# Optimization experiments

Hardware: AMD Instinct MI355X
Metric: run time of the kernel (lower is better)

Reference implementation:

```python
import jax, jax.numpy as jnp
import numpy as np

N_NODES = 100000
N_EDGES = 1200000
N_GRAPHS = 256
IN_C, HID_C, OUT_C = 5, 64, 2


def gcn_conv(x, src, dst, W, b, n_nodes):
    """PyG GCNConv: h = x@W; add self-loops; deg from target col (edge weight 1);
    norm = deg^{-1/2}[src]*deg^{-1/2}[dst]; scatter-add messages into dst; + bias."""
    loop = jnp.arange(n_nodes, dtype=src.dtype)
    s = jnp.concatenate([src, loop])
    d = jnp.concatenate([dst, loop])
    deg = jax.ops.segment_sum(jnp.ones_like(d, dtype=x.dtype), d, num_segments=n_nodes)
    dinv = jnp.where(deg > 0, jax.lax.rsqrt(deg), 0.0)
    norm = dinv[s] * dinv[d]                     # [E+N]
    h = x @ W                                    # [N, out]
    msg = h[s] * norm[:, None]                   # gather + scale  [E+N, out]
    out = jax.ops.segment_sum(msg, d, num_segments=n_nodes)  # scatter-add
    return out + b


def setup_inputs() -> dict:
    key = jax.random.key(0)
    ks = jax.random.split(key, 10)
    x = jax.random.normal(ks[0], (N_NODES, IN_C), dtype=jnp.float32)
    edge_index = jax.random.randint(ks[1], (2, N_EDGES), 0, N_NODES, dtype=jnp.int64)
    batch = jnp.sort(jax.random.randint(ks[2], (N_NODES,), 0, N_GRAPHS, dtype=jnp.int64))
    def glorot(k, fan_in, fan_out):
        lim = np.sqrt(6.0 / (fan_in + fan_out))
        return jax.random.uniform(k, (fan_in, fan_out), jnp.float32, -lim, lim)
    W1 = glorot(ks[3], IN_C, HID_C)
    b1 = jnp.zeros((HID_C,), jnp.float32)
    W2 = glorot(ks[4], HID_C, HID_C)
    b2 = jnp.zeros((HID_C,), jnp.float32)
    Wfc = glorot(ks[5], HID_C, OUT_C)
    bfc = jnp.zeros((OUT_C,), jnp.float32)
    return {"x": x, "edge_index": edge_index, "batch": batch,
            "W1": W1, "b1": b1, "W2": W2, "b2": b2, "Wfc": Wfc, "bfc": bfc}


def reference(x, edge_index, batch, W1, b1, W2, b2, Wfc, bfc):
    src, dst = edge_index[0], edge_index[1]
    h = jax.nn.relu(gcn_conv(x, src, dst, W1, b1, N_NODES))
    h = jax.nn.relu(gcn_conv(h, src, dst, W2, b2, N_NODES))
    # global_mean_pool over graph ids in `batch`
    sums = jax.ops.segment_sum(h, batch, num_segments=N_GRAPHS)          # [G, H]
    cnts = jax.ops.segment_sum(jnp.ones((h.shape[0],), h.dtype), batch,
                               num_segments=N_GRAPHS)                    # [G]
    pooled = sums / jnp.maximum(cnts, 1.0)[:, None]
    return pooled @ Wfc + bfc                                            # [G, 2]
```

## Files before the change

kernel.cpp:

```cpp
#include <hip/hip_runtime.h>

#define N_NODES 100000
#define N_EDGES 1200000
#define N_GRAPHS 256
#define IN_C 5
#define HID_C 64
#define OUT_C 2

#define BSH 7
#define BNODES 128
#define NB ((N_NODES + BNODES - 1) / BNODES)
#define CAPB 2048
#define EPB 2048
#define NCHUNK ((N_EDGES + EPB - 1) / EPB)
#define SEGS 784
#define GNPW 8
#define L1NPW 8

typedef unsigned int uint32;

__device__ __forceinline__ uint32 f2bf(float f) {
    uint32 x = __float_as_uint(f);
    return (x + 0x7FFFu + ((x >> 16) & 1u)) >> 16;
}
__device__ __forceinline__ float bflo(uint32 r) { return __uint_as_float(r << 16); }
__device__ __forceinline__ float bfhi(uint32 r) { return __uint_as_float(r & 0xFFFF0000u); }

__global__ void k_csort(const int* __restrict__ src, const int* __restrict__ dst,
                        int* __restrict__ pairs, int* __restrict__ seg,
                        float* __restrict__ pooled) {
    __shared__ int sp[EPB];
    __shared__ int hist[782];
    __shared__ int st[256];
    int c = blockIdx.x, t = threadIdx.x;
    if (c < (N_GRAPHS * HID_C) / 256)
        pooled[c * 256 + t] = 0.f;
    for (int i = t; i < 782; i += 256) hist[i] = 0;
    __syncthreads();
    int e0 = c * EPB;
    int n = N_EDGES - e0; if (n > EPB) n = EPB;
    int pk[8], bk[8];
#pragma unroll
    for (int i = 0; i < 8; ++i) {
        int idx = t + i * 256;
        if (idx < n) {
            int d = dst[e0 + idx];
            bk[i] = d >> BSH;
            pk[i] = ((d & (BNODES - 1)) << 17) | src[e0 + idx];
            atomicAdd(&hist[bk[i]], 1);
        } else bk[i] = -1;
    }
    __syncthreads();
    int i0 = t * 4;
    int v0 = (i0 + 0 < 782) ? hist[i0 + 0] : 0;
    int v1 = (i0 + 1 < 782) ? hist[i0 + 1] : 0;
    int v2 = (i0 + 2 < 782) ? hist[i0 + 2] : 0;
    int v3 = (i0 + 3 < 782) ? hist[i0 + 3] : 0;
    st[t] = v0 + v1 + v2 + v3;
    __syncthreads();
    for (int off = 1; off < 256; off <<= 1) {
        int a = (t >= off) ? st[t - off] : 0;
        __syncthreads();
        st[t] += a;
        __syncthreads();
    }
    int run = (t > 0) ? st[t - 1] : 0;
    if (i0 + 0 < 782) { hist[i0 + 0] = run; seg[c * SEGS + i0 + 0] = run; run += v0; }
    if (i0 + 1 < 782) { hist[i0 + 1] = run; seg[c * SEGS + i0 + 1] = run; run += v1; }
    if (i0 + 2 < 782) { hist[i0 + 2] = run; seg[c * SEGS + i0 + 2] = run; run += v2; }
    if (i0 + 3 < 782) { hist[i0 + 3] = run; seg[c * SEGS + i0 + 3] = run; run += v3; }
    if (t == 0) seg[c * SEGS + 782] = n;
    __syncthreads();
#pragma unroll
    for (int i = 0; i < 8; ++i)
        if (bk[i] >= 0) {
            int pos = atomicAdd(&hist[bk[i]], 1);
            sp[pos] = pk[i];
        }
    __syncthreads();
    for (int i = t; i < n; i += 256)
        pairs[c * EPB + i] = sp[i];
}

__global__ void k_bsort_xs(const int* __restrict__ pairs, const int* __restrict__ seg,
                           const float* __restrict__ x,
                           int* __restrict__ csr, int* __restrict__ rs,
                           int* __restrict__ cnt, float* __restrict__ dinv,
                           float* __restrict__ xs) {
    __shared__ int spairs[CAPB];
    __shared__ int ssorted[CAPB];
    __shared__ int cid[CAPB];
    __shared__ int ssrc[NCHUNK];
    __shared__ int sdst[NCHUNK];
    __shared__ int st[512];
    __shared__ int hist[BNODES];
    __shared__ int tmp[BNODES];
    __shared__ int cur[BNODES];
    __shared__ float sdv[BNODES];
    int b = blockIdx.x;
    int t = threadIdx.x;
    int base = b << BSH;
    for (int c = t; c < NCHUNK; c += 512) {
        int s0 = seg[c * SEGS + b];
        int s1 = seg[c * SEGS + b + 1];
        sdst[c] = s1 - s0;
        ssrc[c] = c * EPB + s0;
    }
    for (int i = t; i < CAPB; i += 512) cid[i] = -1;
    if (t < BNODES) hist[t] = 0;
    __syncthreads();
    int i0 = 2 * t;
    int v0 = (i0 < NCHUNK) ? sdst[i0] : 0;
    int v1 = (i0 + 1 < NCHUNK) ? sdst[i0 + 1] : 0;
    st[t] = v0 + v1;
    __syncthreads();
    for (int off = 1; off < 512; off <<= 1) {
        int a = (t >= off) ? st[t - off] : 0;
        __syncthreads();
        st[t] += a;
        __syncthreads();
    }
    int run = (t > 0) ? st[t - 1] : 0;
    int n = st[511];
    if (n > CAPB) n = CAPB;
    __syncthreads();
    int s0n = run, s1n = run + v0;
    if (i0 < NCHUNK) sdst[i0] = s0n;
    if (i0 + 1 < NCHUNK) sdst[i0 + 1] = s1n;
    if (i0 < NCHUNK && v0 > 0 && s0n < CAPB) cid[s0n] = i0;
    if (i0 + 1 < NCHUNK && v1 > 0 && s1n < CAPB) cid[s1n] = i0 + 1;
    __syncthreads();
    int sb = 4 * t;
    int m0 = cid[sb];
    int m1 = max(m0, cid[sb + 1]);
    int m2 = max(m1, cid[sb + 2]);
    int m3 = max(m2, cid[sb + 3]);
    __syncthreads();
    st[t] = m3;
    __syncthreads();
    for (int off = 1; off < 512; off <<= 1) {
        int a = (t >= off) ? st[t - off] : -1;
        __syncthreads();
        st[t] = max(st[t], a);
        __syncthreads();
    }
    int excl = (t > 0) ? st[t - 1] : -1;
    int c0 = max(excl, m0), c1 = max(excl, m1);
    int c2 = max(excl, m2), c3 = max(excl, m3);
    int p0 = 0, p1 = 0, p2 = 0, p3 = 0;
    int g0v = (sb + 0 < n), g1v = (sb + 1 < n), g2v = (sb + 2 < n), g3v = (sb + 3 < n);
    if (g0v) p0 = pairs[ssrc[c0] + (sb + 0 - sdst[c0])];
    if (g1v) p1 = pairs[ssrc[c1] + (sb + 1 - sdst[c1])];
    if (g2v) p2 = pairs[ssrc[c2] + (sb + 2 - sdst[c2])];
    if (g3v) p3 = pairs[ssrc[c3] + (sb + 3 - sdst[c3])];
    if (g0v) { spairs[sb + 0] = p0; atomicAdd(&hist[p0 >> 17], 1); }
    if (g1v) { spairs[sb + 1] = p1; atomicAdd(&hist[p1 >> 17], 1); }
    if (g2v) { spairs[sb + 2] = p2; atomicAdd(&hist[p2 >> 17], 1); }
    if (g3v) { spairs[sb + 3] = p3; atomicAdd(&hist[p3 >> 17], 1); }
    __syncthreads();
    int v = (t < BNODES) ? hist[t] : 0;
    if (t < BNODES) tmp[t] = v;
    __syncthreads();
    for (int off = 1; off < BNODES; off <<= 1) {
        int a = (t < BNODES && t >= off) ? tmp[t - off] : 0;
        __syncthreads();
        if (t < BNODES) tmp[t] += a;
        __syncthreads();
    }
    float dv_t = rsqrtf((float)v + 1.0f);
    int s = b << 11;
    if (t < BNODES) {
        cur[t] = tmp[t] - v;
        sdv[t] = dv_t;
        if (base + t < N_NODES) {
            rs[base + t] = s + tmp[t] - v;
            cnt[base + t] = v;
            dinv[base + t] = dv_t;
        }
    }
    __syncthreads();
    for (int i = t; i < n; i += 512) {
        int p = spairs[i];
        int pos = atomicAdd(&cur[p >> 17], 1);
        ssorted[pos] = p & 0x1FFFF;
    }
    __syncthreads();
    for (int i = t; i < n; i += 512)
        csr[s + i] = ssorted[i];
    for (int i = t; i < BNODES * 8; i += 512) {
        int nl = i >> 3, k = i & 7;
        int node = base + nl;
        if (node < N_NODES && k < IN_C)
            xs[(unsigned)node * 8 + k] = x[(unsigned)node * IN_C + k] * sdv[nl];
    }
}

__global__ void __launch_bounds__(256) k_l1(
        const float* __restrict__ xs, const int* __restrict__ csr,
        const int* __restrict__ rs, const int* __restrict__ cnt,
        const float* __restrict__ dinv, const float* __restrict__ b1,
        const float* __restrict__ W1, const float* __restrict__ W2,
        uint32* __restrict__ g2t) {
    __shared__ __align__(16) float sagg[4][L1NPW][8];
    __shared__ __align__(16) float srow[4][2][HID_C];
    int tid = threadIdx.x;
    int w = tid >> 6;
    int lane = tid & 63;
    int base = (blockIdx.x * 4 + w) * L1NPW;

    int g = lane >> 3, l = lane & 7;
    int v = base + g;
    float a0 = 0.f, a1 = 0.f, a2 = 0.f, a3 = 0.f, a4 = 0.f;
    if (v < N_NODES) {
        int k0 = rs[v];
        int n = cnt[v];
        if (l == 0) {
            float4 p = *(const float4*)&xs[(unsigned)v * 8];
            a0 = p.x; a1 = p.y; a2 = p.z; a3 = p.w;
            a4 = xs[(unsigned)v * 8 + 4];
        }
        int i = l;
        int un = (i < n) ? csr[k0 + i] : -1;
        while (un >= 0) {
            int u = un;
            i += 8;
            un = (i < n) ? csr[k0 + i] : -1;
            float4 p = *(const float4*)&xs[(unsigned)u * 8];
            float p4 = xs[(unsigned)u * 8 + 4];
            a0 += p.x; a1 += p.y; a2 += p.z; a3 += p.w; a4 += p4;
        }
    }
#pragma unroll
    for (int off = 4; off; off >>= 1) {
        a0 += __shfl_xor(a0, off);
        a1 += __shfl_xor(a1, off);
        a2 += __shfl_xor(a2, off);
        a3 += __shfl_xor(a3, off);
        a4 += __shfl_xor(a4, off);
    }
    if (l == 0 && v < N_NODES) {
        *(float4*)&sagg[w][g][0] = make_float4(a0, a1, a2, a3);
        sagg[w][g][4] = a4;
    }

    int half = lane >> 5, c2 = lane & 31;
    int kb = half << 5;
    float2 w1r[IN_C];
#pragma unroll
    for (int k = 0; k < IN_C; ++k)
        w1r[k] = *(const float2*)&W1[k * HID_C + 2 * c2];
    float2 w2r[32];
#pragma unroll
    for (int j = 0; j < 32; ++j)
        w2r[j] = *(const float2*)&W2[(kb + j) * HID_C + 2 * c2];
    float2 bias = *(const float2*)&b1[2 * c2];

    for (int gg = 0; gg < L1NPW; ++gg) {
        int node = base + gg;
        if (node >= N_NODES) break;
        float dv = dinv[node];
        float4 qa = *(const float4*)&sagg[w][gg][0];
        float q4 = sagg[w][gg][4];
        float s0 = qa.x * w1r[0].x + qa.y * w1r[1].x + qa.z * w1r[2].x
                 + qa.w * w1r[3].x + q4 * w1r[4].x;
        float s1 = qa.x * w1r[0].y + qa.y * w1r[1].y + qa.z * w1r[2].y
                 + qa.w * w1r[3].y + q4 * w1r[4].y;
        float h0 = fmaxf(s0 * dv + bias.x, 0.f);
        float h1 = fmaxf(s1 * dv + bias.y, 0.f);
        int buf = gg & 1;
        if (half == 0) *(float2*)&srow[w][buf][2 * c2] = make_float2(h0, h1);
        float t0 = 0.f, t1 = 0.f;
#pragma unroll
        for (int jj = 0; jj < 8; ++jj) {
            float4 hv = *(const float4*)&srow[w][buf][kb + 4 * jj];
            t0 += hv.x * w2r[4 * jj + 0].x + hv.y * w2r[4 * jj + 1].x
                + hv.z * w2r[4 * jj + 2].x + hv.w * w2r[4 * jj + 3].x;
            t1 += hv.x * w2r[4 * jj + 0].y + hv.y * w2r[4 * jj + 1].y
                + hv.z * w2r[4 * jj + 2].y + hv.w * w2r[4 * jj + 3].y;
        }
        t0 += __shfl_xor(t0, 32);
        t1 += __shfl_xor(t1, 32);
        if (half == 0)
            g2t[(unsigned)node * 32 + c2] = (f2bf(t1 * dv) << 16) | f2bf(t0 * dv);
    }
}

#define LDU2(d, u) uint2 d = *(const uint2*)&g[(unsigned)(u) * 32 + 2 * c4]
#define ACC4(s0, s1, s2, s3, r) { s0 += bflo(r.x); s1 += bfhi(r.x); \
                                  s2 += bflo(r.y); s3 += bfhi(r.y); }
__global__ void __launch_bounds__(256, 4) k_gather2p(
        const uint32* __restrict__ g, const int* __restrict__ csr,
        const int* __restrict__ rs, const int* __restrict__ cnt,
        const float* __restrict__ dinv, const float* __restrict__ b,
        const int* __restrict__ batch, float* __restrict__ pooled) {
    int wv = __builtin_amdgcn_readfirstlane(
        blockIdx.x * (blockDim.x >> 6) + (threadIdx.x >> 6));
    int n0 = wv * GNPW;
    if (n0 >= N_NODES) return;
    int lane = threadIdx.x & 63;
    int sub = lane >> 4;
    int c4 = lane & 15;
    int va = n0 + sub, vb = n0 + 4 + sub;
    int ka = rs[va], na = cnt[va];
    int kb = rs[vb], nb = cnt[vb];
    float dva = dinv[va], dvb = dinv[vb];
    int ga = batch[va], gb = batch[vb];
    float4 bias = *(const float4*)&b[4 * c4];
    LDU2(rsa, va); LDU2(rsb, vb);
    float a0 = bflo(rsa.x), a1 = bfhi(rsa.x), a2 = bflo(rsa.y), a3 = bfhi(rsa.y);
    float y0 = bflo(rsb.x), y1 = bfhi(rsb.x), y2 = bflo(rsb.y), y3 = bfhi(rsb.y);
    int ia = 0, ib = 0;
    while (ia + 7 < na && ib + 7 < nb) {
        int u0 = csr[ka+ia+0], u1 = csr[ka+ia+1], u2 = csr[ka+ia+2], u3 = csr[ka+ia+3];
        int u4 = csr[ka+ia+4], u5 = csr[ka+ia+5], u6 = csr[ka+ia+6], u7 = csr[ka+ia+7];
        int w0 = csr[kb+ib+0], w1 = csr[kb+ib+1], w2 = csr[kb+ib+2], w3 = csr[kb+ib+3];
        int w4 = csr[kb+ib+4], w5 = csr[kb+ib+5], w6 = csr[kb+ib+6], w7 = csr[kb+ib+7];
        LDU2(p0, u0); LDU2(p1, u1); LDU2(p2, u2); LDU2(p3, u3);
        LDU2(p4, u4); LDU2(p5, u5); LDU2(p6, u6); LDU2(p7, u7);
        LDU2(q0, w0); LDU2(q1, w1); LDU2(q2, w2); LDU2(q3, w3);
        LDU2(q4, w4); LDU2(q5, w5); LDU2(q6, w6); LDU2(q7, w7);
        ACC4(a0, a1, a2, a3, p0); ACC4(a0, a1, a2, a3, p1);
        ACC4(a0, a1, a2, a3, p2); ACC4(a0, a1, a2, a3, p3);
        ACC4(a0, a1, a2, a3, p4); ACC4(a0, a1, a2, a3, p5);
        ACC4(a0, a1, a2, a3, p6); ACC4(a0, a1, a2, a3, p7);
        ACC4(y0, y1, y2, y3, q0); ACC4(y0, y1, y2, y3, q1);
        ACC4(y0, y1, y2, y3, q2); ACC4(y0, y1, y2, y3, q3);
        ACC4(y0, y1, y2, y3, q4); ACC4(y0, y1, y2, y3, q5);
        ACC4(y0, y1, y2, y3, q6); ACC4(y0, y1, y2, y3, q7);
        ia += 8; ib += 8;
    }
    while (ia + 7 < na) {
        int u0 = csr[ka+ia+0], u1 = csr[ka+ia+1], u2 = csr[ka+ia+2], u3 = csr[ka+ia+3];
        int u4 = csr[ka+ia+4], u5 = csr[ka+ia+5], u6 = csr[ka+ia+6], u7 = csr[ka+ia+7];
        LDU2(p0, u0); LDU2(p1, u1); LDU2(p2, u2); LDU2(p3, u3);
        LDU2(p4, u4); LDU2(p5, u5); LDU2(p6, u6); LDU2(p7, u7);
        ACC4(a0, a1, a2, a3, p0); ACC4(a0, a1, a2, a3, p1);
        ACC4(a0, a1, a2, a3, p2); ACC4(a0, a1, a2, a3, p3);
        ACC4(a0, a1, a2, a3, p4); ACC4(a0, a1, a2, a3, p5);
        ACC4(a0, a1, a2, a3, p6); ACC4(a0, a1, a2, a3, p7);
        ia += 8;
    }
    while (ib + 7 < nb) {
        int w0 = csr[kb+ib+0], w1 = csr[kb+ib+1], w2 = csr[kb+ib+2], w3 = csr[kb+ib+3];
        int w4 = csr[kb+ib+4], w5 = csr[kb+ib+5], w6 = csr[kb+ib+6], w7 = csr[kb+ib+7];
        LDU2(q0, w0); LDU2(q1, w1); LDU2(q2, w2); LDU2(q3, w3);
        LDU2(q4, w4); LDU2(q5, w5); LDU2(q6, w6); LDU2(q7, w7);
        ACC4(y0, y1, y2, y3, q0); ACC4(y0, y1, y2, y3, q1);
        ACC4(y0, y1, y2, y3, q2); ACC4(y0, y1, y2, y3, q3);
        ACC4(y0, y1, y2, y3, q4); ACC4(y0, y1, y2, y3, q5);
        ACC4(y0, y1, y2, y3, q6); ACC4(y0, y1, y2, y3, q7);
        ib += 8;
    }
    while (ia + 3 < na && ib + 3 < nb) {
        int u0 = csr[ka+ia+0], u1 = csr[ka+ia+1], u2 = csr[ka+ia+2], u3 = csr[ka+ia+3];
        int w0 = csr[kb+ib+0], w1 = csr[kb+ib+1], w2 = csr[kb+ib+2], w3 = csr[kb+ib+3];
        LDU2(p0, u0); LDU2(p1, u1); LDU2(p2, u2); LDU2(p3, u3);
        LDU2(q0, w0); LDU2(q1, w1); LDU2(q2, w2); LDU2(q3, w3);
        ACC4(a0, a1, a2, a3, p0); ACC4(a0, a1, a2, a3, p1);
        ACC4(a0, a1, a2, a3, p2); ACC4(a0, a1, a2, a3, p3);
        ACC4(y0, y1, y2, y3, q0); ACC4(y0, y1, y2, y3, q1);
        ACC4(y0, y1, y2, y3, q2); ACC4(y0, y1, y2, y3, q3);
        ia += 4; ib += 4;
    }
    while (ia + 3 < na) {
        int u0 = csr[ka+ia+0], u1 = csr[ka+ia+1], u2 = csr[ka+ia+2], u3 = csr[ka+ia+3];
        LDU2(p0, u0); LDU2(p1, u1); LDU2(p2, u2); LDU2(p3, u3);
        ACC4(a0, a1, a2, a3, p0); ACC4(a0, a1, a2, a3, p1);
        ACC4(a0, a1, a2, a3, p2); ACC4(a0, a1, a2, a3, p3);
        ia += 4;
    }
    while (ib + 3 < nb) {
        int w0 = csr[kb+ib+0], w1 = csr[kb+ib+1], w2 = csr[kb+ib+2], w3 = csr[kb+ib+3];
        LDU2(q0, w0); LDU2(q1, w1); LDU2(q2, w2); LDU2(q3, w3);
        ACC4(y0, y1, y2, y3, q0); ACC4(y0, y1, y2, y3, q1);
        ACC4(y0, y1, y2, y3, q2); ACC4(y0, y1, y2, y3, q3);
        ib += 4;
    }
    while (ia < na && ib < nb) {
        int u0 = csr[ka + ia], w0 = csr[kb + ib];
        LDU2(p0, u0); LDU2(q0, w0);
        ACC4(a0, a1, a2, a3, p0); ACC4(y0, y1, y2, y3, q0);
        ++ia; ++ib;
    }
    while (ia < na) {
        LDU2(p0, csr[ka + ia]);
        ACC4(a0, a1, a2, a3, p0);
        ++ia;
    }
    while (ib < nb) {
        LDU2(q0, csr[kb + ib]);
        ACC4(y0, y1, y2, y3, q0);
        ++ib;
    }
    float oa0 = fmaxf(a0 * dva + bias.x, 0.f);
    float oa1 = fmaxf(a1 * dva + bias.y, 0.f);
    float oa2 = fmaxf(a2 * dva + bias.z, 0.f);
    float oa3 = fmaxf(a3 * dva + bias.w, 0.f);
    float ob0 = fmaxf(y0 * dvb + bias.x, 0.f);
    float ob1 = fmaxf(y1 * dvb + bias.y, 0.f);
    float ob2 = fmaxf(y2 * dvb + bias.z, 0.f);
    float ob3 = fmaxf(y3 * dvb + bias.w, 0.f);
    int g0 = __builtin_amdgcn_readfirstlane(ga);
    if (__all(ga == g0) && __all(gb == g0)) {
        float f0 = oa0 + ob0, f1 = oa1 + ob1, f2 = oa2 + ob2, f3 = oa3 + ob3;
        f0 += __shfl_xor(f0, 16); f0 += __shfl_xor(f0, 32);
        f1 += __shfl_xor(f1, 16); f1 += __shfl_xor(f1, 32);
        f2 += __shfl_xor(f2, 16); f2 += __shfl_xor(f2, 32);
        f3 += __shfl_xor(f3, 16); f3 += __shfl_xor(f3, 32);
        if (sub == 0) {
            atomicAdd(&pooled[g0 * HID_C + 4 * c4 + 0], f0);
            atomicAdd(&pooled[g0 * HID_C + 4 * c4 + 1], f1);
            atomicAdd(&pooled[g0 * HID_C + 4 * c4 + 2], f2);
            atomicAdd(&pooled[g0 * HID_C + 4 * c4 + 3], f3);
        }
    } else {
        atomicAdd(&pooled[ga * HID_C + 4 * c4 + 0], oa0);
        atomicAdd(&pooled[ga * HID_C + 4 * c4 + 1], oa1);
        atomicAdd(&pooled[ga * HID_C + 4 * c4 + 2], oa2);
        atomicAdd(&pooled[ga * HID_C + 4 * c4 + 3], oa3);
        atomicAdd(&pooled[gb * HID_C + 4 * c4 + 0], ob0);
        atomicAdd(&pooled[gb * HID_C + 4 * c4 + 1], ob1);
        atomicAdd(&pooled[gb * HID_C + 4 * c4 + 2], ob2);
        atomicAdd(&pooled[gb * HID_C + 4 * c4 + 3], ob3);
    }
}

__global__ void k_fc(const float* __restrict__ pooled, const int* __restrict__ batch,
                     const float* __restrict__ Wfc, const float* __restrict__ bfc,
                     float* __restrict__ out) {
    int g = blockIdx.x;
    int c = threadIdx.x;
    int lo = 0, hi = N_NODES;
    while (lo < hi) { int mid = (lo + hi) >> 1; if (batch[mid] < g) lo = mid + 1; else hi = mid; }
    int start = lo;
    hi = N_NODES;
    while (lo < hi) { int mid = (lo + hi) >> 1; if (batch[mid] < g + 1) lo = mid + 1; else hi = mid; }
    int n = lo - start;
    float pv = pooled[g * HID_C + c] / (float)(n > 0 ? n : 1);
    float o0 = pv * Wfc[c * OUT_C + 0];
    float o1 = pv * Wfc[c * OUT_C + 1];
#pragma unroll
    for (int off = 32; off > 0; off >>= 1) {
        o0 += __shfl_down(o0, off);
        o1 += __shfl_down(o1, off);
    }
    if (c == 0) {
        out[g * OUT_C + 0] = o0 + bfc[0];
        out[g * OUT_C + 1] = o1 + bfc[1];
    }
}

extern "C" void kernel_launch(void* const* d_in, const int* in_sizes, int n_in,
                              void* d_out, int out_size, void* d_ws, size_t ws_size,
                              hipStream_t stream) {
    const float* x    = (const float*)d_in[0];
    const int*   ei   = (const int*)d_in[1];
    const int*   src  = ei;
    const int*   dst  = ei + N_EDGES;
    const int*   batch= (const int*)d_in[2];
    const float* W1   = (const float*)d_in[3];
    const float* b1   = (const float*)d_in[4];
    const float* W2   = (const float*)d_in[5];
    const float* b2   = (const float*)d_in[6];
    const float* Wfc  = (const float*)d_in[7];
    const float* bfc  = (const float*)d_in[8];
    float* out = (float*)d_out;

    float*  ws     = (float*)d_ws;
    float*  pooled = ws;
    float*  dinv   = ws + 16384;
    int*    cnt    = (int*)(dinv + 100352);
    int*    rs     = cnt + 100352;
    int*    seg    = rs + 100352;
    int*    pairs  = seg + NCHUNK * SEGS;
    int*    csr    = pairs + NCHUNK * EPB;
    float*  xs     = (float*)(csr + NB * CAPB);
    uint32* g2tab  = (uint32*)(xs + N_NODES * 8);

    k_csort<<<NCHUNK, 256, 0, stream>>>(src, dst, pairs, seg, pooled);
    k_bsort_xs<<<NB, 512, 0, stream>>>(pairs, seg, x, csr, rs, cnt, dinv, xs);

    {
        int blocks = (N_NODES + 4 * L1NPW - 1) / (4 * L1NPW);
        k_l1<<<blocks, 256, 0, stream>>>(xs, csr, rs, cnt, dinv, b1, W1, W2, g2tab);
    }

    {
        int waves = (N_NODES + GNPW - 1) / GNPW;
        int blocks = (waves + 3) / 4;
        k_gather2p<<<blocks, 256, 0, stream>>>(g2tab, csr, rs, cnt, dinv, b2, batch, pooled);
    }

    k_fc<<<N_GRAPHS, 64, 0, stream>>>(pooled, batch, Wfc, bfc, out);
}
```

Baseline: 189.6 us.

## Use wave-shuffle scans and transpose segment offsets for coalesced bucket reads

Replaces the shared-memory Hillis-Steele prefix scans, which need many block barriers, with wave-level __shfl_up scans plus a small per-wave sum array in both sort kernels. Adds a kernel that transposes the per-chunk segment offset table so that k_bsort_xs reads its offsets contiguously instead of with stride SEGS. The aim is fewer barriers and better-coalesced global reads, at the cost of an extra launch and a second copy of the offset table.

```diff
diff --git a/kernel.cpp b/kernel.cpp
--- a/kernel.cpp
+++ b/kernel.cpp
@@ -14,6 +14,7 @@
 #define EPB 2048
 #define NCHUNK ((N_EDGES + EPB - 1) / EPB)
 #define SEGS 784
+#define NCP 592
 #define GNPW 8
 #define L1NPW 8
 
@@ -31,7 +32,7 @@
                         float* __restrict__ pooled) {
     __shared__ int sp[EPB];
     __shared__ int hist[782];
-    __shared__ int st[256];
+    __shared__ int wsum[4];
     int c = blockIdx.x, t = threadIdx.x;
     if (c < (N_GRAPHS * HID_C) / 256)
         pooled[c * 256 + t] = 0.f;
@@ -56,15 +57,19 @@
     int v1 = (i0 + 1 < 782) ? hist[i0 + 1] : 0;
     int v2 = (i0 + 2 < 782) ? hist[i0 + 2] : 0;
     int v3 = (i0 + 3 < 782) ? hist[i0 + 3] : 0;
-    st[t] = v0 + v1 + v2 + v3;
-    __syncthreads();
-    for (int off = 1; off < 256; off <<= 1) {
-        int a = (t >= off) ? st[t - off] : 0;
-        __syncthreads();
-        st[t] += a;
-        __syncthreads();
-    }
-    int run = (t > 0) ? st[t - 1] : 0;
+    int sv = v0 + v1 + v2 + v3;
+    int lane = t & 63, wid = t >> 6;
+    int inc = sv;
+#pragma unroll
+    for (int off = 1; off < 64; off <<= 1) {
+        int up = __shfl_up(inc, off);
+        if (lane >= off) inc += up;
+    }
+    if (lane == 63) wsum[wid] = inc;
+    __syncthreads();
+    int wof = 0;
+    for (int wv = 0; wv < wid; ++wv) wof += wsum[wv];
+    int run = wof + inc - sv;
     if (i0 + 0 < 782) { hist[i0 + 0] = run; seg[c * SEGS + i0 + 0] = run; run += v0; }
     if (i0 + 1 < 782) { hist[i0 + 1] = run; seg[c * SEGS + i0 + 1] = run; run += v1; }
     if (i0 + 2 < 782) { hist[i0 + 2] = run; seg[c * SEGS + i0 + 2] = run; run += v2; }
@@ -82,7 +87,22 @@
         pairs[c * EPB + i] = sp[i];
 }
 
-__global__ void k_bsort_xs(const int* __restrict__ pairs, const int* __restrict__ seg,
+__global__ void k_segT(const int* __restrict__ seg, int* __restrict__ segT) {
+    __shared__ int tile[32][33];
+    int b0 = blockIdx.x * 32, c0 = blockIdx.y * 32;
+    int tx = threadIdx.x, ty = threadIdx.y;
+    for (int j = ty; j < 32; j += 8) {
+        int c = c0 + j, b = b0 + tx;
+        tile[j][tx] = (c < NCHUNK && b < SEGS) ? seg[c * SEGS + b] : 0;
+    }
+    __syncthreads();
+    for (int j = ty; j < 32; j += 8) {
+        int b = b0 + j, c = c0 + tx;
+        if (b < SEGS && c < NCP) segT[(unsigned)b * NCP + c] = tile[tx][j];
+    }
+}
+
+__global__ void k_bsort_xs(const int* __restrict__ pairs, const int* __restrict__ segT,
                            const float* __restrict__ x,
                            int* __restrict__ csr, int* __restrict__ rs,
                            int* __restrict__ cnt, float* __restrict__ dinv,
@@ -92,17 +112,17 @@
     __shared__ int cid[CAPB];
     __shared__ int ssrc[NCHUNK];
     __shared__ int sdst[NCHUNK];
-    __shared__ int st[512];
+    __shared__ int wsum[8];
     __shared__ int hist[BNODES];
-    __shared__ int tmp[BNODES];
     __shared__ int cur[BNODES];
     __shared__ float sdv[BNODES];
     int b = blockIdx.x;
     int t = threadIdx.x;
+    int lane = t & 63, wid = t >> 6;
     int base = b << BSH;
     for (int c = t; c < NCHUNK; c += 512) {
-        int s0 = seg[c * SEGS + b];
-        int s1 = seg[c * SEGS + b + 1];
+        int s0 = segT[(unsigned)b * NCP + c];
+        int s1 = segT[(unsigned)(b + 1) * NCP + c];
         sdst[c] = s1 - s0;
         ssrc[c] = c * EPB + s0;
     }
@@ -112,18 +132,25 @@
     int i0 = 2 * t;
     int v0 = (i0 < NCHUNK) ? sdst[i0] : 0;
     int v1 = (i0 + 1 < NCHUNK) ? sdst[i0 + 1] : 0;
-    st[t] = v0 + v1;
-    __syncthreads();
-    for (int off = 1; off < 512; off <<= 1) {
-        int a = (t >= off) ? st[t - off] : 0;
-        __syncthreads();
-        st[t] += a;
-        __syncthreads();
-    }
-    int run = (t > 0) ? st[t - 1] : 0;
-    int n = st[511];
+    int sv = v0 + v1;
+    int inc = sv;
+#pragma unroll
+    for (int off = 1; off < 64; off <<= 1) {
+        int up = __shfl_up(inc, off);
+        if (lane >= off) inc += up;
+    }
+    if (lane == 63) wsum[wid] = inc;
+    __syncthreads();
+    int wof = 0, total = 0;
+#pragma unroll
+    for (int wv = 0; wv < 8; ++wv) {
+        int s = wsum[wv];
+        if (wv < wid) wof += s;
+        total += s;
+    }
+    int run = wof + inc - sv;
+    int n = total;
     if (n > CAPB) n = CAPB;
-    __syncthreads();
     int s0n = run, s1n = run + v0;
     if (i0 < NCHUNK) sdst[i0] = s0n;
     if (i0 + 1 < NCHUNK) sdst[i0 + 1] = s1n;
@@ -135,16 +162,18 @@
     int m1 = max(m0, cid[sb + 1]);
     int m2 = max(m1, cid[sb + 2]);
     int m3 = max(m2, cid[sb + 3]);
-    __syncthreads();
-    st[t] = m3;
-    __syncthreads();
-    for (int off = 1; off < 512; off <<= 1) {
-        int a = (t >= off) ? st[t - off] : -1;
-        __syncthreads();
-        st[t] = max(st[t], a);
-        __syncthreads();
-    }
-    int excl = (t > 0) ? st[t - 1] : -1;
+    int incm = m3;
+#pragma unroll
+    for (int off = 1; off < 64; off <<= 1) {
+        int up = __shfl_up(incm, off);
+        if (lane >= off) incm = max(incm, up);
+    }
+    if (lane == 63) wsum[wid] = incm;
+    __syncthreads();
+    int wofm = -1;
+    for (int wv = 0; wv < wid; ++wv) wofm = max(wofm, wsum[wv]);
+    int prev = __shfl_up(incm, 1);
+    int excl = max(wofm, (lane >= 1) ? prev : -1);
     int c0 = max(excl, m0), c1 = max(excl, m1);
     int c2 = max(excl, m2), c3 = max(excl, m3);
     int p0 = 0, p1 = 0, p2 = 0, p3 = 0;
@@ -159,21 +188,22 @@
     if (g3v) { spairs[sb + 3] = p3; atomicAdd(&hist[p3 >> 17], 1); }
     __syncthreads();
     int v = (t < BNODES) ? hist[t] : 0;
-    if (t < BNODES) tmp[t] = v;
-    __syncthreads();
-    for (int off = 1; off < BNODES; off <<= 1) {
-        int a = (t < BNODES && t >= off) ? tmp[t - off] : 0;
-        __syncthreads();
-        if (t < BNODES) tmp[t] += a;
-        __syncthreads();
-    }
+    int inc3 = v;
+#pragma unroll
+    for (int off = 1; off < 64; off <<= 1) {
+        int up = __shfl_up(inc3, off);
+        if (lane >= off) inc3 += up;
+    }
+    if (t < BNODES && lane == 63) wsum[wid] = inc3;
+    __syncthreads();
     float dv_t = rsqrtf((float)v + 1.0f);
     int s = b << 11;
     if (t < BNODES) {
-        cur[t] = tmp[t] - v;
+        int tot_incl = inc3 + ((wid == 1) ? wsum[0] : 0);
+        cur[t] = tot_incl - v;
         sdv[t] = dv_t;
         if (base + t < N_NODES) {
-            rs[base + t] = s + tmp[t] - v;
+            rs[base + t] = s + tot_incl - v;
             cnt[base + t] = v;
             dinv[base + t] = dv_t;
         }
@@ -472,13 +502,18 @@
     int*    cnt    = (int*)(dinv + 100352);
     int*    rs     = cnt + 100352;
     int*    seg    = rs + 100352;
-    int*    pairs  = seg + NCHUNK * SEGS;
+    int*    segT   = seg + NCHUNK * SEGS;
+    int*    pairs  = segT + SEGS * NCP;
     int*    csr    = pairs + NCHUNK * EPB;
     float*  xs     = (float*)(csr + NB * CAPB);
     uint32* g2tab  = (uint32*)(xs + N_NODES * 8);
 
     k_csort<<<NCHUNK, 256, 0, stream>>>(src, dst, pairs, seg, pooled);
-    k_bsort_xs<<<NB, 512, 0, stream>>>(pairs, seg, x, csr, rs, cnt, dinv, xs);
+    {
+        dim3 tgrid((SEGS + 31) / 32, (NCHUNK + 31) / 32);
+        k_segT<<<tgrid, dim3(32, 8), 0, stream>>>(seg, segT);
+    }
+    k_bsort_xs<<<NB, 512, 0, stream>>>(pairs, segT, x, csr, rs, cnt, dinv, xs);
 
     {
         int blocks = (N_NODES + 4 * L1NPW - 1) / (4 * L1NPW);
```

New measurement: 188.3 us. No clear change (-0.7%).
